# Kernel optimization log

Hardware: AMD Instinct MI355X
Metric: run time of the kernel (lower is better)

## Reference

```python
import jax, jax.numpy as jnp
import numpy as np

N = 50000       # num_nodes
E = 800000      # num_edges (avg degree 16)
DIN = 128       # input_dim
DOUT = 128      # output_dim
H = 4           # num_heads
HD = DOUT // H  # head_dim = 32


def setup_inputs() -> dict:
    key = jax.random.key(0)
    ks = jax.random.split(key, 9)
    x = jax.random.normal(ks[0], (N, DIN), dtype=jnp.float32)
    edge_index = jax.random.randint(ks[1], (2, E), 0, N, dtype=jnp.int64)
    s = 1.0 / np.sqrt(DIN)
    Wq = jax.random.uniform(ks[2], (DOUT, DIN), jnp.float32, -s, s)
    bq = jax.random.uniform(ks[3], (DOUT,), jnp.float32, -s, s)
    Wk = jax.random.uniform(ks[4], (DOUT, DIN), jnp.float32, -s, s)
    bk = jax.random.uniform(ks[5], (DOUT,), jnp.float32, -s, s)
    Wv = jax.random.uniform(ks[6], (DOUT, DIN), jnp.float32, -s, s)
    bv = jax.random.uniform(ks[7], (DOUT,), jnp.float32, -s, s)
    att = jax.random.normal(ks[8], (H, 2 * HD), dtype=jnp.float32)  # nn.Parameter(randn)
    return {"x": x, "edge_index": edge_index, "Wq": Wq, "bq": bq,
            "Wk": Wk, "bk": bk, "Wv": Wv, "bv": bv, "att": att}


def reference(x, edge_index, Wq, bq, Wk, bk, Wv, bv, att):
    n = x.shape[0]
    q = (x @ Wq.T + bq).reshape(n, H, HD)
    k = (x @ Wk.T + bk).reshape(n, H, HD)
    v = (x @ Wv.T + bv).reshape(n, H, HD)
    row, col = edge_index[0], edge_index[1]

    # scores = leaky_relu(sum(cat([q[row],k[col]]) * att)) computed without concat
    a_q, a_k = att[:, :HD], att[:, HD:]                       # [H,HD] each
    scores = jnp.einsum('ehd,hd->eh', q[row], a_q) \
           + jnp.einsum('ehd,hd->eh', k[col], a_k)            # [E,H]
    scores = jax.nn.leaky_relu(scores, 0.2)

    # segment-softmax over edges grouped by destination node (col), per head
    m = jax.ops.segment_max(scores, col, num_segments=n)      # [N,H]
    m = jnp.where(jnp.isfinite(m), m, 0.0)                    # empty segments -> -inf guard
    e = jnp.exp(scores - m[col])                              # [E,H]
    denom = jax.ops.segment_sum(e, col, num_segments=n)       # [N,H]
    w_edge = e / denom[col]                                   # softmax per dst segment

    # attention_weights[i] = mean over incoming edges of softmax weights; 0 if deg==0
    deg = jax.ops.segment_sum(jnp.ones((col.shape[0],), jnp.float32), col,
                              num_segments=n)                 # [N]
    w_sum = jax.ops.segment_sum(w_edge, col, num_segments=n)  # [N,H]
    attn_w = jnp.where(deg[:, None] > 0, w_sum / jnp.maximum(deg, 1.0)[:, None], 0.0)

    # output[dst] += attn_w[dst] * v[src], summed over edges
    msgs = attn_w[col][:, :, None] * v[row]                   # [E,H,HD]
    out = jax.ops.segment_sum(msgs, col, num_segments=n)      # [N,H,HD]
    return out.reshape(n, DOUT)                               # dropout: eval mode (identity)
```

## Files before the change

kernel.cpp:

```cpp
#include <hip/hip_runtime.h>


#define N_NODES 50000
#define N_EDGES 800000
#define SPAN    96
#define NBUCK   521
#define CAP     2304
#define HSPAN   48
#define EPB     2048
#define NCHUNK  391
#define GEMMB   391

#define OFF_SORTED 12800000
#define OFF_CURSOR 17601536

typedef __attribute__((ext_vector_type(8))) short short8;
typedef __attribute__((ext_vector_type(4))) float f32x4;

__device__ __forceinline__ unsigned int pack_bf16_rne(float a, float b) {
    unsigned int ua = __float_as_uint(a), ub = __float_as_uint(b);
    unsigned int ha = (ua + 0x7FFFu + ((ua >> 16) & 1u)) >> 16;
    unsigned int hb = (ub + 0x7FFFu + ((ub >> 16) & 1u)) >> 16;
    return ha | (hb << 16);
}
__device__ __forceinline__ unsigned short bf16_rne(float a) {
    unsigned int ua = __float_as_uint(a);
    return (unsigned short)((ua + 0x7FFFu + ((ua >> 16) & 1u)) >> 16);
}
__device__ __forceinline__ float bflo(unsigned int u) { return __uint_as_float(u << 16); }
__device__ __forceinline__ float bfhi(unsigned int u) { return __uint_as_float(u & 0xFFFF0000u); }

__global__ __launch_bounds__(512) void fused_gemm_scatter(
        const float* __restrict__ x, const float* __restrict__ Wv,
        const float* __restrict__ bv, unsigned int* __restrict__ vh,
        const int* __restrict__ ei, unsigned int* __restrict__ Cursor,
        unsigned int* __restrict__ sorted) {
    __shared__ __align__(16) unsigned char smem[128 * 68 * 4];
    __shared__ int s_wide;
    int t = threadIdx.x;

    if (blockIdx.x < GEMMB) {
        unsigned int* wB = (unsigned int*)smem;
        for (int q = t; q < 8192; q += 512) {
            int o = q >> 6, k2 = q & 63;
            float2 wp = ((const float2*)Wv)[q];
            wB[o * 68 + k2] = pack_bf16_rne(wp.x, wp.y);
        }
        __syncthreads();

        int lane = t & 63, w = t >> 6;
        int quad = lane >> 4, lc = lane & 15;
        int n0 = blockIdx.x * 128 + w * 16;

        int arow = n0 + lc;
        int arowc = min(arow, N_NODES - 1);
        const float4* xrow = (const float4*)(x + (size_t)arowc * 128);

        f32x4 acc[8];
        #pragma unroll
        for (int ot = 0; ot < 8; ++ot) acc[ot] = (f32x4){0.f, 0.f, 0.f, 0.f};

        #pragma unroll
        for (int ks = 0; ks < 4; ++ks) {
            float4 f0 = xrow[ks * 8 + quad * 2];
            float4 f1 = xrow[ks * 8 + quad * 2 + 1];
            uint4 a4;
            a4.x = pack_bf16_rne(f0.x, f0.y);
            a4.y = pack_bf16_rne(f0.z, f0.w);
            a4.z = pack_bf16_rne(f1.x, f1.y);
            a4.w = pack_bf16_rne(f1.z, f1.w);
            short8 af = *(const short8*)&a4;
            #pragma unroll
            for (int ot = 0; ot < 8; ++ot) {
                uint4 b4 = *(const uint4*)&wB[(ot * 16 + lc) * 68 + ks * 16 + quad * 4];
                short8 bf = *(const short8*)&b4;
                acc[ot] = __builtin_amdgcn_mfma_f32_16x16x32_bf16(af, bf, acc[ot], 0, 0, 0);
            }
        }

        #pragma unroll
        for (int ot = 0; ot < 8; ++ot) {
            int o = ot * 16 + lc;
            float bb = bv[o];
            #pragma unroll
            for (int r = 0; r < 4; ++r) {
                int node = n0 + quad * 4 + r;
                unsigned short u = bf16_rne(acc[ot][r] + bb);
                unsigned int partner = (unsigned int)__shfl_xor((int)u, 1, 64);
                if ((lane & 1) == 0 && node < N_NODES) {
                    unsigned int pair = (unsigned int)u | (partner << 16);
                    vh[(size_t)node * 64 + (o >> 1)] = pair;
                }
            }
        }
    } else {
        unsigned int* w = (unsigned int*)smem;
        int* h    = (int*)(smem + EPB * 4);
        int* base = (int*)(smem + EPB * 4 + NBUCK * 4);
        unsigned int V = Cursor[NBUCK];
        for (int j = t; j < NBUCK; j += 512) h[j] = 0;
        if (t < 64) {
            int nz = (ei[2 * t + 1] != 0) ? 1 : 0;
            unsigned long long b = __ballot(nz);
            if (t == 0) s_wide = (b == 0ULL) ? 1 : 0;
        }
        __syncthreads();
        int wide = s_wide;
        int e0 = (blockIdx.x - GEMMB) * EPB;

        #pragma unroll
        for (int k = 0; k < EPB / 512; ++k) {
            int e = e0 + k * 512 + t;
            if (e < N_EDGES) {
                int r, c;
                if (wide) {
                    r = (int)((const uint2*)ei)[e].x;
                    c = (int)((const uint2*)ei)[N_EDGES + e].x;
                } else {
                    r = ei[e];
                    c = ei[N_EDGES + e];
                }
                w[k * 512 + t] = ((unsigned int)c << 16) | (unsigned int)r;
                atomicAdd(&h[c / SPAN], 1);
            } else {
                w[k * 512 + t] = 0xFFFFFFFFu;
            }
        }
        __syncthreads();
        for (int j = t; j < NBUCK; j += 512) {
            int cnt = h[j];
            base[j] = cnt ? (int)(atomicAdd(&Cursor[j], (unsigned int)cnt) - V) : 0;
            h[j] = 0;
        }
        __syncthreads();
        #pragma unroll
        for (int k = 0; k < EPB / 512; ++k) {
            unsigned int ww = w[k * 512 + t];
            if (ww != 0xFFFFFFFFu) {
                int bin = (int)(ww >> 16) / SPAN;
                int p = base[bin] + atomicAdd(&h[bin], 1);
                if (p >= 0 && p < CAP)
                    sorted[(size_t)bin * CAP + p] = ww;
            }
        }
    }
}

__global__ __launch_bounds__(512) void gather_kernel(const unsigned int* __restrict__ vh,
                                                     const unsigned int* __restrict__ sorted,
                                                     const unsigned int* __restrict__ Cursor,
                                                     float* __restrict__ out) {
    __shared__ unsigned int ww[CAP];
    __shared__ unsigned short rl[CAP];
    __shared__ int deg[HSPAN];
    __shared__ int startc[HSPAN];
    __shared__ int curp[HSPAN];
    int t = threadIdx.x;
    int b  = blockIdx.x >> 1;
    int hb = blockIdx.x & 1;
    int nb0 = b * SPAN + hb * HSPAN;
    int span = min(HSPAN, N_NODES - nb0);
    if (span <= 0) return;
    unsigned int V = Cursor[NBUCK];
    int cnt = min((int)(Cursor[b] - V), CAP);
    if (t < HSPAN) deg[t] = 0;
    __syncthreads();

    const unsigned int* run = sorted + (size_t)b * CAP;
    for (int i = t; i < cnt; i += 512) {
        unsigned int v = run[i];
        ww[i] = v;
        unsigned int ln = (v >> 16) - (unsigned int)nb0;
        if (ln < (unsigned int)HSPAN) atomicAdd(&deg[ln], 1);
    }
    __syncthreads();

    if (t < 64) {
        int v = (t < HSPAN) ? deg[t] : 0;
        int s = v;
        #pragma unroll
        for (int off = 1; off < 64; off <<= 1) {
            int y = __shfl_up(s, off, 64);
            if (t >= off) s += y;
        }
        if (t < HSPAN) { startc[t] = s - v; curp[t] = 0; }
    }
    __syncthreads();

    for (int i = t; i < cnt; i += 512) {
        unsigned int v = ww[i];
        unsigned int ln = (v >> 16) - (unsigned int)nb0;
        if (ln < (unsigned int)HSPAN) {
            int p = startc[ln] + atomicAdd(&curp[ln], 1);
            rl[p] = (unsigned short)(v & 0xFFFFu);
        }
    }
    __syncthreads();

    int lane = t & 63, wid = t >> 6;
    int quad = lane >> 4;
    int li = lane & 15;
    const uint4* v4 = (const uint4*)vh;

#define ACC8(p) do { \
        c0 += (double)bflo((p).x); c1 += (double)bfhi((p).x); \
        c2 += (double)bflo((p).y); c3 += (double)bfhi((p).y); \
        c4 += (double)bflo((p).z); c5 += (double)bfhi((p).z); \
        c6 += (double)bflo((p).w); c7 += (double)bfhi((p).w); } while (0)

    for (int g = wid; g * 4 < span; g += 8) {
        int ln = g * 4 + quad;
        int s0 = startc[ln], d = deg[ln];
        double c0 = 0., c1 = 0., c2 = 0., c3 = 0.;
        double c4 = 0., c5 = 0., c6 = 0., c7 = 0.;
        int j = 0;
        if (d >= 8) {
            int a0 = rl[s0 + 0], a1 = rl[s0 + 1];
            int a2 = rl[s0 + 2], a3 = rl[s0 + 3];
            uint4 pA0 = v4[(size_t)a0 * 16 + li];
            uint4 pA1 = v4[(size_t)a1 * 16 + li];
            uint4 pA2 = v4[(size_t)a2 * 16 + li];
            uint4 pA3 = v4[(size_t)a3 * 16 + li];
            for (; j + 8 <= d; j += 4) {
                int b0 = rl[s0 + j + 4], b1 = rl[s0 + j + 5];
                int b2 = rl[s0 + j + 6], b3 = rl[s0 + j + 7];
                uint4 pB0 = v4[(size_t)b0 * 16 + li];
                uint4 pB1 = v4[(size_t)b1 * 16 + li];
                uint4 pB2 = v4[(size_t)b2 * 16 + li];
                uint4 pB3 = v4[(size_t)b3 * 16 + li];
                ACC8(pA0); ACC8(pA1); ACC8(pA2); ACC8(pA3);
                pA0 = pB0; pA1 = pB1; pA2 = pB2; pA3 = pB3;
            }
            ACC8(pA0); ACC8(pA1); ACC8(pA2); ACC8(pA3);
            j += 4;
        } else if (d >= 4) {
            int a0 = rl[s0 + 0], a1 = rl[s0 + 1];
            int a2 = rl[s0 + 2], a3 = rl[s0 + 3];
            uint4 pA0 = v4[(size_t)a0 * 16 + li];
            uint4 pA1 = v4[(size_t)a1 * 16 + li];
            uint4 pA2 = v4[(size_t)a2 * 16 + li];
            uint4 pA3 = v4[(size_t)a3 * 16 + li];
            ACC8(pA0); ACC8(pA1); ACC8(pA2); ACC8(pA3);
            j = 4;
        }
        for (; j < d; ++j) {
            int r0 = rl[s0 + j];
            uint4 p0 = v4[(size_t)r0 * 16 + li];
            ACC8(p0);
        }
        double sc = (d > 0) ? 1.0 / (double)d : 0.0;
        float4 ra = {(float)(c0 * sc), (float)(c1 * sc),
                     (float)(c2 * sc), (float)(c3 * sc)};
        float4 rb = {(float)(c4 * sc), (float)(c5 * sc),
                     (float)(c6 * sc), (float)(c7 * sc)};
        ((float4*)out)[(size_t)(nb0 + ln) * 32 + 2 * li]     = ra;
        ((float4*)out)[(size_t)(nb0 + ln) * 32 + 2 * li + 1] = rb;
    }
#undef ACC8
}

extern "C" void kernel_launch(void* const* d_in, const int* in_sizes, int n_in,
                              void* d_out, int out_size, void* d_ws, size_t ws_size,
                              hipStream_t stream) {
    const float* x  = (const float*)d_in[0];
    const int*   ei = (const int*)d_in[1];
    const float* Wv = (const float*)d_in[6];
    const float* bv = (const float*)d_in[7];
    float* out = (float*)d_out;

    char* ws = (char*)d_ws;
    unsigned int* vh     = (unsigned int*)(ws);
    unsigned int* sorted = (unsigned int*)(ws + OFF_SORTED);
    unsigned int* Cursor = (unsigned int*)(ws + OFF_CURSOR);

    fused_gemm_scatter<<<GEMMB + NCHUNK, 512, 0, stream>>>(x, Wv, bv, vh,
                                                           ei, Cursor, sorted);
    gather_kernel<<<NBUCK * 2, 512, 0, stream>>>(vh, sorted, Cursor, out);
}
```

Baseline: 139.4 us.

## Split gather into two feature-half launches to cut register pressure

```diff
diff --git a/kernel.cpp b/kernel.cpp
--- a/kernel.cpp
+++ b/kernel.cpp
@@ -149,7 +149,8 @@
 __global__ __launch_bounds__(512) void gather_kernel(const unsigned int* __restrict__ vh,
                                                      const unsigned int* __restrict__ sorted,
                                                      const unsigned int* __restrict__ Cursor,
-                                                     float* __restrict__ out) {
+                                                     float* __restrict__ out,
+                                                     int ch) {
     __shared__ unsigned int ww[CAP];
     __shared__ unsigned short rl[CAP];
     __shared__ int deg[HSPAN];
@@ -200,63 +201,57 @@
     int lane = t & 63, wid = t >> 6;
     int quad = lane >> 4;
     int li = lane & 15;
-    const uint4* v4 = (const uint4*)vh;
-
-#define ACC8(p) do { \
+    const uint2* v2 = (const uint2*)(vh + (size_t)ch * 32);
+
+#define ACC4(p) do { \
         c0 += (double)bflo((p).x); c1 += (double)bfhi((p).x); \
-        c2 += (double)bflo((p).y); c3 += (double)bfhi((p).y); \
-        c4 += (double)bflo((p).z); c5 += (double)bfhi((p).z); \
-        c6 += (double)bflo((p).w); c7 += (double)bfhi((p).w); } while (0)
+        c2 += (double)bflo((p).y); c3 += (double)bfhi((p).y); } while (0)
 
     for (int g = wid; g * 4 < span; g += 8) {
         int ln = g * 4 + quad;
         int s0 = startc[ln], d = deg[ln];
         double c0 = 0., c1 = 0., c2 = 0., c3 = 0.;
-        double c4 = 0., c5 = 0., c6 = 0., c7 = 0.;
         int j = 0;
         if (d >= 8) {
             int a0 = rl[s0 + 0], a1 = rl[s0 + 1];
             int a2 = rl[s0 + 2], a3 = rl[s0 + 3];
-            uint4 pA0 = v4[(size_t)a0 * 16 + li];
-            uint4 pA1 = v4[(size_t)a1 * 16 + li];
-            uint4 pA2 = v4[(size_t)a2 * 16 + li];
-            uint4 pA3 = v4[(size_t)a3 * 16 + li];
+            uint2 pA0 = v2[(size_t)a0 * 32 + li];
+            uint2 pA1 = v2[(size_t)a1 * 32 + li];
+            uint2 pA2 = v2[(size_t)a2 * 32 + li];
+            uint2 pA3 = v2[(size_t)a3 * 32 + li];
             for (; j + 8 <= d; j += 4) {
                 int b0 = rl[s0 + j + 4], b1 = rl[s0 + j + 5];
                 int b2 = rl[s0 + j + 6], b3 = rl[s0 + j + 7];
-                uint4 pB0 = v4[(size_t)b0 * 16 + li];
-                uint4 pB1 = v4[(size_t)b1 * 16 + li];
-                uint4 pB2 = v4[(size_t)b2 * 16 + li];
-                uint4 pB3 = v4[(size_t)b3 * 16 + li];
-                ACC8(pA0); ACC8(pA1); ACC8(pA2); ACC8(pA3);
+                uint2 pB0 = v2[(size_t)b0 * 32 + li];
+                uint2 pB1 = v2[(size_t)b1 * 32 + li];
+                uint2 pB2 = v2[(size_t)b2 * 32 + li];
+                uint2 pB3 = v2[(size_t)b3 * 32 + li];
+                ACC4(pA0); ACC4(pA1); ACC4(pA2); ACC4(pA3);
                 pA0 = pB0; pA1 = pB1; pA2 = pB2; pA3 = pB3;
             }
-            ACC8(pA0); ACC8(pA1); ACC8(pA2); ACC8(pA3);
+            ACC4(pA0); ACC4(pA1); ACC4(pA2); ACC4(pA3);
             j += 4;
         } else if (d >= 4) {
             int a0 = rl[s0 + 0], a1 = rl[s0 + 1];
             int a2 = rl[s0 + 2], a3 = rl[s0 + 3];
-            uint4 pA0 = v4[(size_t)a0 * 16 + li];
-            uint4 pA1 = v4[(size_t)a1 * 16 + li];
-            uint4 pA2 = v4[(size_t)a2 * 16 + li];
-            uint4 pA3 = v4[(size_t)a3 * 16 + li];
-            ACC8(pA0); ACC8(pA1); ACC8(pA2); ACC8(pA3);
+            uint2 pA0 = v2[(size_t)a0 * 32 + li];
+            uint2 pA1 = v2[(size_t)a1 * 32 + li];
+            uint2 pA2 = v2[(size_t)a2 * 32 + li];
+            uint2 pA3 = v2[(size_t)a3 * 32 + li];
+            ACC4(pA0); ACC4(pA1); ACC4(pA2); ACC4(pA3);
             j = 4;
         }
         for (; j < d; ++j) {
             int r0 = rl[s0 + j];
-            uint4 p0 = v4[(size_t)r0 * 16 + li];
-            ACC8(p0);
+            uint2 p0 = v2[(size_t)r0 * 32 + li];
+            ACC4(p0);
         }
         double sc = (d > 0) ? 1.0 / (double)d : 0.0;
         float4 ra = {(float)(c0 * sc), (float)(c1 * sc),
                      (float)(c2 * sc), (float)(c3 * sc)};
-        float4 rb = {(float)(c4 * sc), (float)(c5 * sc),
-                     (float)(c6 * sc), (float)(c7 * sc)};
-        ((float4*)out)[(size_t)(nb0 + ln) * 32 + 2 * li]     = ra;
-        ((float4*)out)[(size_t)(nb0 + ln) * 32 + 2 * li + 1] = rb;
-    }
-#undef ACC8
+        ((float4*)out)[(size_t)(nb0 + ln) * 32 + ch * 16 + li] = ra;
+    }
+#undef ACC4
 }
 
 extern "C" void kernel_launch(void* const* d_in, const int* in_sizes, int n_in,
@@ -275,5 +270,6 @@
 
     fused_gemm_scatter<<<GEMMB + NCHUNK, 512, 0, stream>>>(x, Wv, bv, vh,
                                                            ei, Cursor, sorted);
-    gather_kernel<<<NBUCK * 2, 512, 0, stream>>>(vh, sorted, Cursor, out);
-}
+    gather_kernel<<<NBUCK * 2, 512, 0, stream>>>(vh, sorted, Cursor, out, 0);
+    gather_kernel<<<NBUCK * 2, 512, 0, stream>>>(vh, sorted, Cursor, out, 1);
+}
```

New measurement: 150.2 us. 1.08x slower.
